# Kernel optimization log

Measured on AMD Instinct MI355X. Metric: run time of the kernel, lower is better.

## Reference

```python
import jax, jax.numpy as jnp
import numpy as np

B, N, F_IN, F_OUT = 8, 2048, 512, 512


def setup_inputs() -> dict:
    key = jax.random.key(0)
    k1, k2, k3, k4 = jax.random.split(key, 4)
    X = jax.random.normal(k1, (B, N, F_IN), dtype=jnp.float32)
    A = jax.random.uniform(k2, (B, N, N), dtype=jnp.float32)
    # nn.Linear params (kaiming-uniform-ish scale is irrelevant for correctness)
    bound = 1.0 / np.sqrt(F_IN)
    W = jax.random.uniform(k3, (F_IN, F_OUT), dtype=jnp.float32, minval=-bound, maxval=bound)
    b = jax.random.uniform(k4, (F_OUT,), dtype=jnp.float32, minval=-bound, maxval=bound)
    return {"X": X, "A": A, "W": W, "b": b}


def reference(X, A, W, b):
    # A' = A + I  (self-loops)
    A_hat = A + jnp.eye(A.shape[-1], dtype=A.dtype)
    # D^{-1/2}: per-row degree of A'.  torch builds diag_embed + two bmms;
    # mathematically identical to broadcasted row/column scaling.
    d_inv_sqrt = A_hat.sum(axis=-1) ** -0.5                      # [B, N]
    L = A_hat * d_inv_sqrt[:, :, None] * d_inv_sqrt[:, None, :]  # [B, N, N]
    x = X @ W + b                                                # [B, N, F_out]
    return jnp.einsum('bij,bjf->bif', L, x)
```

## Files before the change

### kernel.cpp

```cpp
#include <hip/hip_runtime.h>

#define B_ 8
#define N_ 2048
#define FIN_ 512
#define FOUT_ 512

typedef __attribute__((ext_vector_type(8))) short short8;
typedef __attribute__((ext_vector_type(4))) float floatx4;
typedef __attribute__((ext_vector_type(4))) unsigned short ushortx4;
typedef __attribute__((ext_vector_type(8))) unsigned short ushortx8;

__device__ inline unsigned short f2bf(float f) {
    union { float f; unsigned int u; } x; x.f = f;
    unsigned int r = x.u + 0x7FFFu + ((x.u >> 16) & 1u);
    return (unsigned short)(r >> 16);
}

__device__ inline void glds16(const void* g, void* l) {
    __builtin_amdgcn_global_load_lds(
        (const __attribute__((address_space(1))) void*)g,
        (__attribute__((address_space(3))) void*)l, 16, 0, 0);
}

__global__ __launch_bounds__(256) void degree_kernel(const float* __restrict__ A,
                                                     float* __restrict__ dinv) {
    int row = blockIdx.x;
    const float4* A4 = (const float4*)(A + (size_t)row * N_);
    int t = threadIdx.x;
    float4 v0 = A4[t];
    float4 v1 = A4[t + 256];
    float s = v0.x + v0.y + v0.z + v0.w + v1.x + v1.y + v1.z + v1.w;
#pragma unroll
    for (int off = 32; off > 0; off >>= 1) s += __shfl_down(s, off, 64);
    __shared__ float red[4];
    if ((t & 63) == 0) red[t >> 6] = s;
    __syncthreads();
    if (t == 0) dinv[row] = rsqrtf(red[0] + red[1] + red[2] + red[3] + 1.0f);
}

__global__ __launch_bounds__(256) void scaleL_kernel(const float* __restrict__ A,
                                                     const float* __restrict__ dinv,
                                                     unsigned short* __restrict__ Lbf) {
    size_t e0 = ((size_t)blockIdx.x * 256 + threadIdx.x) * 8;
    int b   = (int)(e0 >> 22);
    int rem = (int)(e0 & ((1u << 22) - 1));
    int i   = rem >> 11;
    int j0  = rem & 2047;
    float di = dinv[b * N_ + i];
    const float* dj = dinv + b * N_ + j0;
    float4 a0 = *(const float4*)(A + e0);
    float4 a1 = *(const float4*)(A + e0 + 4);
    float4 d0 = *(const float4*)(dj);
    float4 d1 = *(const float4*)(dj + 4);
    float av[8] = {a0.x, a0.y, a0.z, a0.w, a1.x, a1.y, a1.z, a1.w};
    float dv[8] = {d0.x, d0.y, d0.z, d0.w, d1.x, d1.y, d1.z, d1.w};
    int dd = i - j0;
    if (dd >= 0 && dd < 8) av[dd] += 1.0f;
    ushortx8 p;
#pragma unroll
    for (int r = 0; r < 8; ++r) p[r] = f2bf(av[r] * di * dv[r]);
    *(ushortx8*)(Lbf + e0) = p;
}

__global__ __launch_bounds__(256) void castX_kernel(const float* __restrict__ X,
                                                    unsigned short* __restrict__ Xbf) {
    size_t e0 = ((size_t)blockIdx.x * 256 + threadIdx.x) * 8;
    float4 a0 = *(const float4*)(X + e0);
    float4 a1 = *(const float4*)(X + e0 + 4);
    float av[8] = {a0.x, a0.y, a0.z, a0.w, a1.x, a1.y, a1.z, a1.w};
    ushortx8 p;
#pragma unroll
    for (int r = 0; r < 8; ++r) p[r] = f2bf(av[r]);
    *(ushortx8*)(Xbf + e0) = p;
}

__global__ __launch_bounds__(256) void transposeW_kernel(const float* __restrict__ W,
                                                         unsigned short* __restrict__ Wt) {
    __shared__ float tile[32][33];
    int bx = blockIdx.x * 32;
    int by = blockIdx.y * 32;
    int tx = threadIdx.x, ty = threadIdx.y;
#pragma unroll
    for (int r = 0; r < 32; r += 8)
        tile[ty + r][tx] = W[(size_t)(by + ty + r) * FOUT_ + bx + tx];
    __syncthreads();
#pragma unroll
    for (int r = 0; r < 32; r += 8)
        Wt[(size_t)(bx + ty + r) * FIN_ + by + tx] = f2bf(tile[tx][ty + r]);
}

__global__ __launch_bounds__(256) void gemm1_kernel(
    const unsigned short* __restrict__ Abase,
    const unsigned short* __restrict__ Btbase,
    unsigned short* __restrict__ XwT,
    const float* __restrict__ bias) {
    __shared__ __align__(16) char smem[34816];
    char* As = smem;
    char* Bs = smem + 8192;

    int t = threadIdx.x;
    int lane = t & 63;
    int wave = t >> 6;
    int wr = wave >> 1, wc = wave & 1;
    int q = lane >> 4, m = lane & 15;
    int n0 = blockIdx.x * 128;
    int m0 = blockIdx.y * 128;

    int srow = t >> 2;
    int skk = (t & 3) * 8;

    floatx4 acc[4][4];
#pragma unroll
    for (int mi = 0; mi < 4; ++mi)
#pragma unroll
        for (int ni = 0; ni < 4; ++ni)
            acc[mi][ni] = (floatx4){0.f, 0.f, 0.f, 0.f};

    const unsigned short* gA  = Abase + (size_t)(m0 + srow) * FIN_ + skk;
    const unsigned short* gA2 = Abase + (size_t)(m0 + srow + 64) * FIN_ + skk;
    const unsigned short* gB  = Btbase + (size_t)(srow) * FIN_ + skk;
    const unsigned short* gB2 = Btbase + (size_t)(srow + 64) * FIN_ + skk;
    gB  += (size_t)n0 * FIN_;
    gB2 += (size_t)n0 * FIN_;
    char* lA  = As + wave * 1024;
    char* lA2 = As + 4096 + wave * 1024;
    char* lB  = Bs + wave * 1024;
    char* lB2 = Bs + 4096 + wave * 1024;

    for (int kt = 0; kt < FIN_ / 32; ++kt) {
        glds16(gA, lA);
        glds16(gA2, lA2);
        glds16(gB, lB);
        glds16(gB2, lB2);
        gA += 32; gA2 += 32; gB += 32; gB2 += 32;
        __syncthreads();

        short8 af[4], bfr[4];
#pragma unroll
        for (int mi = 0; mi < 4; ++mi)
            af[mi] = *(const short8*)(As + (wr * 64 + mi * 16 + m) * 64 + q * 16);
#pragma unroll
        for (int ni = 0; ni < 4; ++ni)
            bfr[ni] = *(const short8*)(Bs + (wc * 64 + ni * 16 + m) * 64 + q * 16);
#pragma unroll
        for (int mi = 0; mi < 4; ++mi)
#pragma unroll
            for (int ni = 0; ni < 4; ++ni)
                acc[mi][ni] = __builtin_amdgcn_mfma_f32_16x16x32_bf16(
                    af[mi], bfr[ni], acc[mi][ni], 0, 0, 0);
        __syncthreads();
    }

    unsigned short* T = (unsigned short*)smem;
#pragma unroll
    for (int mi = 0; mi < 4; ++mi) {
        int row = wr * 64 + mi * 16 + q * 4;
#pragma unroll
        for (int ni = 0; ni < 4; ++ni) {
            int col = wc * 64 + ni * 16 + m;
            float bv = bias[n0 + col];
            ushortx4 pk;
#pragma unroll
            for (int r = 0; r < 4; ++r) pk[r] = f2bf(acc[mi][ni][r] + bv);
            *(ushortx4*)(T + col * 136 + row) = pk;
        }
    }
    __syncthreads();
    int f  = t >> 1;
    int c0 = (t & 1) * 64;
    int bb = m0 >> 11;
    int node0 = (m0 & 2047) + c0;
    unsigned short* dst = XwT + ((size_t)bb * FOUT_ + n0 + f) * N_ + node0;
    const unsigned short* src = T + f * 136 + c0;
#pragma unroll
    for (int u = 0; u < 8; ++u)
        *(ushortx8*)(dst + u * 8) = *(const ushortx8*)(src + u * 8);
}

__global__ __launch_bounds__(256) void gemm2_kernel(
    const unsigned short* __restrict__ Lbf,
    const unsigned short* __restrict__ XwT,
    float* __restrict__ out) {
    __shared__ __align__(16) char smem[12288];
    char* As = smem;
    char* Bs = smem + 4096;

    int t = threadIdx.x;
    int lane = t & 63;
    int wave = t >> 6;
    int wr = wave & 1;
    int wc = wave >> 1;
    int q = lane >> 4, m = lane & 15;
    int n0 = blockIdx.x * 128;
    int m0 = blockIdx.y * 64;
    int b = blockIdx.z;
    const unsigned short* Ab = Lbf + (size_t)b * N_ * N_;
    const unsigned short* Bb = XwT + (size_t)b * FOUT_ * N_;

    int srow = t >> 2;
    int skk = (t & 3) * 8;

    floatx4 acc[2][4];
#pragma unroll
    for (int mi = 0; mi < 2; ++mi)
#pragma unroll
        for (int ni = 0; ni < 4; ++ni)
            acc[mi][ni] = (floatx4){0.f, 0.f, 0.f, 0.f};

    const unsigned short* gA  = Ab + (size_t)(m0 + srow) * N_ + skk;
    const unsigned short* gB  = Bb + (size_t)(n0 + srow) * N_ + skk;
    const unsigned short* gB2 = Bb + (size_t)(n0 + srow + 64) * N_ + skk;
    char* lA  = As + wave * 1024;
    char* lB  = Bs + wave * 1024;
    char* lB2 = Bs + 4096 + wave * 1024;

    for (int kt = 0; kt < N_ / 32; ++kt) {
        glds16(gA, lA);
        glds16(gB, lB);
        glds16(gB2, lB2);
        gA += 32; gB += 32; gB2 += 32;
        __syncthreads();

        short8 af[2], bfr[4];
#pragma unroll
        for (int mi = 0; mi < 2; ++mi)
            af[mi] = *(const short8*)(As + (wr * 32 + mi * 16 + m) * 64 + q * 16);
#pragma unroll
        for (int ni = 0; ni < 4; ++ni)
            bfr[ni] = *(const short8*)(Bs + (wc * 64 + ni * 16 + m) * 64 + q * 16);
#pragma unroll
        for (int mi = 0; mi < 2; ++mi)
#pragma unroll
            for (int ni = 0; ni < 4; ++ni)
                acc[mi][ni] = __builtin_amdgcn_mfma_f32_16x16x32_bf16(
                    af[mi], bfr[ni], acc[mi][ni], 0, 0, 0);
        __syncthreads();
    }

    float* C = out + (size_t)b * N_ * FOUT_;
#pragma unroll
    for (int mi = 0; mi < 2; ++mi) {
        int rowb = m0 + wr * 32 + mi * 16 + q * 4;
#pragma unroll
        for (int ni = 0; ni < 4; ++ni) {
            int col = n0 + wc * 64 + ni * 16 + m;
#pragma unroll
            for (int r = 0; r < 4; ++r)
                C[(size_t)(rowb + r) * FOUT_ + col] = acc[mi][ni][r];
        }
    }
}

extern "C" void kernel_launch(void* const* d_in, const int* in_sizes, int n_in,
                              void* d_out, int out_size, void* d_ws, size_t ws_size,
                              hipStream_t stream) {
    const float* X    = (const float*)d_in[0];
    const float* A    = (const float*)d_in[1];
    const float* W    = (const float*)d_in[2];
    const float* bias = (const float*)d_in[3];
    float* out = (float*)d_out;
    char* ws = (char*)d_ws;

    float* dinv          = (float*)(ws);
    unsigned short* Xbf  = (unsigned short*)(ws + (1u << 16));
    unsigned short* Wt   = (unsigned short*)(ws + (1u << 16) + 16777216u);
    unsigned short* XwT  = (unsigned short*)(ws + (1u << 16) + 16777216u + 524288u);
    unsigned short* Lbf  = (unsigned short*)(ws + (1u << 16) + 16777216u + 524288u + 16777216u);

    degree_kernel<<<B_ * N_, 256, 0, stream>>>(A, dinv);
    scaleL_kernel<<<(B_ * (size_t)N_ * N_) / 2048, 256, 0, stream>>>(A, dinv, Lbf);
    castX_kernel<<<((size_t)B_ * N_ * FIN_) / 2048, 256, 0, stream>>>(X, Xbf);
    transposeW_kernel<<<dim3(FOUT_ / 32, FIN_ / 32), dim3(32, 8), 0, stream>>>(W, Wt);

    gemm1_kernel<<<dim3(FOUT_ / 128, (B_ * N_) / 128), 256, 0, stream>>>(
        Xbf, Wt, XwT, bias);

    gemm2_kernel<<<dim3(FOUT_ / 128, N_ / 64, B_), 256, 0, stream>>>(
        Lbf, XwT, out);
}
```

Baseline: 344.6 us.

## Double K-tile depth to 64 and XOR-swizzle LDS layout in both GEMMs

Both GEMM kernels now stage 64-wide K slices per iteration instead of 32, halving the number of barrier pairs and loop iterations. The LDS row stride becomes 128 bytes, with an XOR swizzle on the 16-byte chunk index applied consistently to the global-to-LDS loads and the fragment reads, to avoid bank conflicts. LDS usage per block grows, which may reduce occupancy for gemm2. There is still no double buffering, so loads and compute remain serialized per iteration.

```diff
diff --git a/kernel.cpp b/kernel.cpp
--- a/kernel.cpp
+++ b/kernel.cpp
@@ -89,6 +89,7 @@
         Wt[(size_t)(bx + ty + r) * FIN_ + by + tx] = f2bf(tile[tx][ty + r]);
 }
 
+
 __global__ __launch_bounds__(256) void gemm1_kernel(
     const unsigned short* __restrict__ Abase,
     const unsigned short* __restrict__ Btbase,
@@ -96,7 +97,7 @@
     const float* __restrict__ bias) {
     __shared__ __align__(16) char smem[34816];
     char* As = smem;
-    char* Bs = smem + 8192;
+    char* Bs = smem + 16384;
 
     int t = threadIdx.x;
     int lane = t & 63;
@@ -106,8 +107,11 @@
     int n0 = blockIdx.x * 128;
     int m0 = blockIdx.y * 128;
 
-    int srow = t >> 2;
-    int skk = (t & 3) * 8;
+    int srow = t >> 3;
+    int scol = (((t & 7) ^ (srow & 7)) * 8);
+
+    int x0 = ((q ^ (m & 7)) * 16);
+    int x1 = x0 ^ 64;
 
     floatx4 acc[4][4];
 #pragma unroll
@@ -116,38 +120,37 @@
         for (int ni = 0; ni < 4; ++ni)
             acc[mi][ni] = (floatx4){0.f, 0.f, 0.f, 0.f};
 
-    const unsigned short* gA  = Abase + (size_t)(m0 + srow) * FIN_ + skk;
-    const unsigned short* gA2 = Abase + (size_t)(m0 + srow + 64) * FIN_ + skk;
-    const unsigned short* gB  = Btbase + (size_t)(srow) * FIN_ + skk;
-    const unsigned short* gB2 = Btbase + (size_t)(srow + 64) * FIN_ + skk;
-    gB  += (size_t)n0 * FIN_;
-    gB2 += (size_t)n0 * FIN_;
-    char* lA  = As + wave * 1024;
-    char* lA2 = As + 4096 + wave * 1024;
-    char* lB  = Bs + wave * 1024;
-    char* lB2 = Bs + 4096 + wave * 1024;
-
-    for (int kt = 0; kt < FIN_ / 32; ++kt) {
-        glds16(gA, lA);
-        glds16(gA2, lA2);
-        glds16(gB, lB);
-        glds16(gB2, lB2);
-        gA += 32; gA2 += 32; gB += 32; gB2 += 32;
-        __syncthreads();
-
-        short8 af[4], bfr[4];
-#pragma unroll
-        for (int mi = 0; mi < 4; ++mi)
-            af[mi] = *(const short8*)(As + (wr * 64 + mi * 16 + m) * 64 + q * 16);
-#pragma unroll
-        for (int ni = 0; ni < 4; ++ni)
-            bfr[ni] = *(const short8*)(Bs + (wc * 64 + ni * 16 + m) * 64 + q * 16);
-#pragma unroll
-        for (int mi = 0; mi < 4; ++mi)
+    const unsigned short* gA = Abase + (size_t)(m0 + srow) * FIN_ + scol;
+    const unsigned short* gB = Btbase + (size_t)(n0 + srow) * FIN_ + scol;
+    char* lA = As + wave * 1024;
+    char* lB = Bs + wave * 1024;
+
+    for (int kt = 0; kt < FIN_ / 64; ++kt) {
+#pragma unroll
+        for (int u = 0; u < 4; ++u) {
+            glds16(gA + (size_t)(u * 32) * FIN_, lA + u * 4096);
+            glds16(gB + (size_t)(u * 32) * FIN_, lB + u * 4096);
+        }
+        gA += 64; gB += 64;
+        __syncthreads();
+
+#pragma unroll
+        for (int s = 0; s < 2; ++s) {
+            int xs = s ? x1 : x0;
+            short8 af[4], bfr[4];
+#pragma unroll
+            for (int mi = 0; mi < 4; ++mi)
+                af[mi] = *(const short8*)(As + (wr * 64 + mi * 16 + m) * 128 + xs);
 #pragma unroll
             for (int ni = 0; ni < 4; ++ni)
-                acc[mi][ni] = __builtin_amdgcn_mfma_f32_16x16x32_bf16(
-                    af[mi], bfr[ni], acc[mi][ni], 0, 0, 0);
+                bfr[ni] = *(const short8*)(Bs + (wc * 64 + ni * 16 + m) * 128 + xs);
+#pragma unroll
+            for (int mi = 0; mi < 4; ++mi)
+#pragma unroll
+                for (int ni = 0; ni < 4; ++ni)
+                    acc[mi][ni] = __builtin_amdgcn_mfma_f32_16x16x32_bf16(
+                        af[mi], bfr[ni], acc[mi][ni], 0, 0, 0);
+        }
         __syncthreads();
     }
 
@@ -181,9 +184,9 @@
     const unsigned short* __restrict__ Lbf,
     const unsigned short* __restrict__ XwT,
     float* __restrict__ out) {
-    __shared__ __align__(16) char smem[12288];
+    __shared__ __align__(16) char smem[24576];
     char* As = smem;
-    char* Bs = smem + 4096;
+    char* Bs = smem + 8192;
 
     int t = threadIdx.x;
     int lane = t & 63;
@@ -197,8 +200,10 @@
     const unsigned short* Ab = Lbf + (size_t)b * N_ * N_;
     const unsigned short* Bb = XwT + (size_t)b * FOUT_ * N_;
 
-    int srow = t >> 2;
-    int skk = (t & 3) * 8;
+    int srow = t >> 3;
+    int scol = (((t & 7) ^ (srow & 7)) * 8);
+    int x0 = ((q ^ (m & 7)) * 16);
+    int x1 = x0 ^ 64;
 
     floatx4 acc[2][4];
 #pragma unroll
@@ -207,33 +212,38 @@
         for (int ni = 0; ni < 4; ++ni)
             acc[mi][ni] = (floatx4){0.f, 0.f, 0.f, 0.f};
 
-    const unsigned short* gA  = Ab + (size_t)(m0 + srow) * N_ + skk;
-    const unsigned short* gB  = Bb + (size_t)(n0 + srow) * N_ + skk;
-    const unsigned short* gB2 = Bb + (size_t)(n0 + srow + 64) * N_ + skk;
-    char* lA  = As + wave * 1024;
-    char* lB  = Bs + wave * 1024;
-    char* lB2 = Bs + 4096 + wave * 1024;
-
-    for (int kt = 0; kt < N_ / 32; ++kt) {
-        glds16(gA, lA);
-        glds16(gB, lB);
-        glds16(gB2, lB2);
-        gA += 32; gB += 32; gB2 += 32;
-        __syncthreads();
-
-        short8 af[2], bfr[4];
-#pragma unroll
-        for (int mi = 0; mi < 2; ++mi)
-            af[mi] = *(const short8*)(As + (wr * 32 + mi * 16 + m) * 64 + q * 16);
-#pragma unroll
-        for (int ni = 0; ni < 4; ++ni)
-            bfr[ni] = *(const short8*)(Bs + (wc * 64 + ni * 16 + m) * 64 + q * 16);
-#pragma unroll
-        for (int mi = 0; mi < 2; ++mi)
+    const unsigned short* gA = Ab + (size_t)(m0 + srow) * N_ + scol;
+    const unsigned short* gB = Bb + (size_t)(n0 + srow) * N_ + scol;
+    char* lA = As + wave * 1024;
+    char* lB = Bs + wave * 1024;
+
+    for (int kt = 0; kt < N_ / 64; ++kt) {
+#pragma unroll
+        for (int u = 0; u < 2; ++u)
+            glds16(gA + (size_t)(u * 32) * N_, lA + u * 4096);
+#pragma unroll
+        for (int u = 0; u < 4; ++u)
+            glds16(gB + (size_t)(u * 32) * N_, lB + u * 4096);
+        gA += 64; gB += 64;
+        __syncthreads();
+
+#pragma unroll
+        for (int s = 0; s < 2; ++s) {
+            int xs = s ? x1 : x0;
+            short8 af[2], bfr[4];
+#pragma unroll
+            for (int mi = 0; mi < 2; ++mi)
+                af[mi] = *(const short8*)(As + (wr * 32 + mi * 16 + m) * 128 + xs);
 #pragma unroll
             for (int ni = 0; ni < 4; ++ni)
-                acc[mi][ni] = __builtin_amdgcn_mfma_f32_16x16x32_bf16(
-                    af[mi], bfr[ni], acc[mi][ni], 0, 0, 0);
+                bfr[ni] = *(const short8*)(Bs + (wc * 64 + ni * 16 + m) * 128 + xs);
+#pragma unroll
+            for (int mi = 0; mi < 2; ++mi)
+#pragma unroll
+                for (int ni = 0; ni < 4; ++ni)
+                    acc[mi][ni] = __builtin_amdgcn_mfma_f32_16x16x32_bf16(
+                        af[mi], bfr[ni], acc[mi][ni], 0, 0, 0);
+        }
         __syncthreads();
     }
 
```

Measured after the change: 344.2 us. No clear change (-0.1%).
